# Optimization experiments

Hardware: AMD Instinct MI355X
Metric: run time of the kernel (lower is better)

## Reference

```python
import jax, jax.numpy as jnp
import numpy as np

N_EMBED = 1024
N_HEAD = 16
SEQ = 2048
BATCH = 2


def setup_inputs() -> dict:
    key = jax.random.key(0)
    ks = jax.random.split(key, 5)
    scale_in = 1.0 / np.sqrt(N_EMBED)
    x = jax.random.normal(ks[0], (BATCH, SEQ, N_EMBED), dtype=jnp.float32)
    # attn_proj: Linear(n_embed, 3*n_embed); stored as [in, out] so y = x @ W + b
    W_qkv = jax.random.normal(ks[1], (N_EMBED, 3 * N_EMBED), dtype=jnp.float32) * scale_in
    b_qkv = jax.random.normal(ks[2], (3 * N_EMBED,), dtype=jnp.float32) * 0.01
    # fin_proj: Linear(n_embed, n_embed)
    W_out = jax.random.normal(ks[3], (N_EMBED, N_EMBED), dtype=jnp.float32) * scale_in
    b_out = jax.random.normal(ks[4], (N_EMBED,), dtype=jnp.float32) * 0.01
    return {"x": x, "W_qkv": W_qkv, "b_qkv": b_qkv, "W_out": W_out, "b_out": b_out}


def reference(x, W_qkv, b_qkv, W_out, b_out):
    B, S, D = x.shape
    H = N_HEAD
    hd = D // H
    qkv = x @ W_qkv + b_qkv  # [B, S, 3D]
    q, k, v = jnp.split(qkv, 3, axis=-1)
    # [B, H, S, hd]
    q = q.reshape(B, S, H, hd).transpose(0, 2, 1, 3)
    k = k.reshape(B, S, H, hd).transpose(0, 2, 1, 3)
    v = v.reshape(B, S, H, hd).transpose(0, 2, 1, 3)
    scores = jnp.einsum("bhqd,bhkd->bhqk", q, k) * (1.0 / np.sqrt(hd))
    causal = jnp.tril(jnp.ones((S, S), dtype=bool))  # lower-triangular mask
    scores = jnp.where(causal[None, None], scores, -jnp.inf)
    probs = jax.nn.softmax(scores, axis=-1)
    # dropout is identity in eval mode (inference reference)
    attn = jnp.einsum("bhqk,bhkd->bhqd", probs, v)  # [B, H, S, hd]
    attn = attn.transpose(0, 2, 1, 3).reshape(B, S, D)
    return attn @ W_out + b_out
```

## Files before the change

kernel.cpp:

```cpp
#include <hip/hip_runtime.h>

typedef short bf16x8 __attribute__((ext_vector_type(8)));
typedef short bf16x4 __attribute__((ext_vector_type(4)));
typedef float f32x4 __attribute__((ext_vector_type(4)));
typedef int i32x4 __attribute__((ext_vector_type(4)));
typedef int i32x2 __attribute__((ext_vector_type(2)));

#define MFMA16x16x32(a, b, c) __builtin_amdgcn_mfma_f32_16x16x32_bf16(a, b, c, 0, 0, 0)
#define TRR(dst, a) asm volatile("ds_read_b64_tr_b16 %0, %1" : "=v"(dst) : "v"(a))

__device__ __forceinline__ unsigned short f2bf(float f) {
  union { float f; unsigned u; } v; v.f = f;
  unsigned u = v.u + 0x7FFFu + ((v.u >> 16) & 1u);
  return (unsigned short)(u >> 16);
}

__device__ __forceinline__ unsigned cvtpk(float lo, float hi) {
  unsigned r;
  asm("v_cvt_pk_bf16_f32 %0, %1, %2" : "=v"(r) : "v"(lo), "v"(hi));
  return r;
}

__device__ __forceinline__ float max3f(float a, float b, float c) {
  float d;
  asm("v_max3_f32 %0, %1, %2, %3" : "=v"(d) : "v"(a), "v"(b), "v"(c));
  return d;
}

__device__ __forceinline__ void gload16(const void* g, void* l) {
  __builtin_amdgcn_global_load_lds((const __attribute__((address_space(1))) void*)g,
                                   (__attribute__((address_space(3))) void*)l, 16, 0, 0);
}

__device__ __forceinline__ unsigned ldsoff(const void* p) {
  return (unsigned)(unsigned long long)(const __attribute__((address_space(3))) void*)p;
}

__global__ __launch_bounds__(256) void conv_bf16(const float* __restrict__ in,
                                                 unsigned short* __restrict__ out, int n8) {
  int i = blockIdx.x * 256 + threadIdx.x;
  if (i >= n8) return;
  const float4* p = reinterpret_cast<const float4*>(in + (long)i * 8);
  float4 a = p[0], b = p[1];
  i32x4 o;
  o[0] = cvtpk(a.x, a.y); o[1] = cvtpk(a.z, a.w);
  o[2] = cvtpk(b.x, b.y); o[3] = cvtpk(b.z, b.w);
  *reinterpret_cast<i32x4*>(out + (long)i * 8) = o;
}

__global__ __launch_bounds__(256) void trans_f32_bf16(const float* __restrict__ W,
                                                      unsigned short* __restrict__ Wt,
                                                      int K, int N) {
  __shared__ float tile[32][33];
  int n0 = blockIdx.x << 5, k0 = blockIdx.y << 5;
  int tx = threadIdx.x, ty = threadIdx.y;
#pragma unroll
  for (int i = 0; i < 32; i += 8)
    tile[ty + i][tx] = W[(long)(k0 + ty + i) * N + n0 + tx];
  __syncthreads();
#pragma unroll
  for (int i = 0; i < 32; i += 8)
    Wt[(long)(n0 + ty + i) * K + k0 + tx] = f2bf(tile[tx][ty + i]);
}

template <int BF16OUT>
__global__ __launch_bounds__(256) void gemm_bt(const unsigned short* __restrict__ A,
                                               const unsigned short* __restrict__ Bt,
                                               const float* __restrict__ bias,
                                               void* __restrict__ Cv,
                                               int M, int N, int K) {
  __shared__ __align__(128) unsigned short As[4096];
  __shared__ __align__(128) unsigned short Bs[4096];
  int t = threadIdx.x;
  int w = t >> 6, l = t & 63;
  int g = l >> 4, m16 = l & 15;
  int wr = w >> 1, wc = w & 1;
  long am0 = (long)blockIdx.y << 7;
  long bn0 = (long)blockIdx.x << 7;
  f32x4 acc[4][4];
#pragma unroll
  for (int i = 0; i < 4; ++i)
#pragma unroll
    for (int j = 0; j < 4; ++j) acc[i][j] = (f32x4){0.f, 0.f, 0.f, 0.f};

  for (int k0 = 0; k0 < K; k0 += 32) {
#pragma unroll
    for (int i = 0; i < 2; ++i) {
      int seg = i * 4 + w;
      int flat = (seg << 9) + (l << 3);
      int r_ = flat >> 5, c_ = flat & 31;
      gload16(A + (am0 + r_) * K + k0 + c_, &As[seg << 9]);
      gload16(Bt + (bn0 + r_) * K + k0 + c_, &Bs[seg << 9]);
    }
    __syncthreads();
    bf16x8 af[4], bfr[4];
#pragma unroll
    for (int im = 0; im < 4; ++im)
      af[im] = *(const bf16x8*)&As[((wr << 6) + (im << 4) + m16) * 32 + (g << 3)];
#pragma unroll
    for (int in = 0; in < 4; ++in)
      bfr[in] = *(const bf16x8*)&Bs[((wc << 6) + (in << 4) + m16) * 32 + (g << 3)];
    __builtin_amdgcn_s_setprio(1);
#pragma unroll
    for (int im = 0; im < 4; ++im)
#pragma unroll
      for (int in = 0; in < 4; ++in)
        acc[im][in] = MFMA16x16x32(af[im], bfr[in], acc[im][in]);
    __builtin_amdgcn_s_setprio(0);
    __syncthreads();
  }

#pragma unroll
  for (int im = 0; im < 4; ++im) {
#pragma unroll
    for (int in = 0; in < 4; ++in) {
      long col = bn0 + (wc << 6) + (in << 4) + m16;
      float bval = bias[col];
#pragma unroll
      for (int r = 0; r < 4; ++r) {
        long row = am0 + (wr << 6) + (im << 4) + (g << 2) + r;
        float v = acc[im][in][r] + bval;
        if (BF16OUT)
          ((unsigned short*)Cv)[row * N + col] = f2bf(v);
        else
          ((float*)Cv)[row * N + col] = v;
      }
    }
  }
}

__global__ __launch_bounds__(256, 2) void attn_fwd(const unsigned short* __restrict__ qkv,
                                                   unsigned short* __restrict__ out) {
  const int D3 = 3072;
  const float C1 = 0.18033688f;
  const float THR = 11.5415603f;
  __shared__ __align__(128) unsigned short Ks[2][8192];
  __shared__ __align__(128) unsigned short Vs[2][8192];
  int b = blockIdx.x >> 4, h = blockIdx.x & 15;
  int t = threadIdx.x;
  int w = t >> 6, l = t & 63;
  int g = l >> 4, m16 = l & 15;
  long base = (long)b * 2048 * D3;
  const unsigned short* kbase = qkv + base + 1024 + h * 64;
  const unsigned short* vbase = qkv + base + 2048 + h * 64;

  int l8 = l >> 3, sc = l & 7;
  int kof = (w * 8 + l8) * D3 + ((sc ^ l8) << 3);
  int vof = ((w * 8 + l8) * 4 + (sc >> 1)) * D3 + ((sc & 1) << 3);
  const f32x4 zero4 = (f32x4){0.f, 0.f, 0.f, 0.f};

  for (int sgi = 0; sgi < 2; ++sgi) {
    int qt = sgi ? (31 - blockIdx.y) : blockIdx.y;
    int q0 = qt << 6;
    int qrow = q0 + (w << 4) + m16;
    const unsigned short* qp = qkv + base + (long)qrow * D3 + h * 64;
    bf16x8 qf0 = *(const bf16x8*)(qp + g * 8);
    bf16x8 qf1 = *(const bf16x8*)(qp + 32 + g * 8);

    f32x4 O[4];
#pragma unroll
    for (int d = 0; d < 4; ++d) O[d] = zero4;
    float m2 = -1e30f, lsum = 0.f;
    int nt = (qt >> 1) + 1;

#pragma unroll
    for (int i = 0; i < 4; ++i) {
      gload16(kbase + kof + i * 32 * D3, &Ks[0][(i << 11) + (w << 9)]);
      gload16(vbase + vof + (i << 4), &Vs[0][(i << 11) + (w << 9)]);
    }
    __syncthreads();

    int buf = 0;
    for (int it = 0; it < nt; ++it) {
      if (it + 1 < nt) {
        long off = (long)(it + 1) * 128 * D3;
#pragma unroll
        for (int i = 0; i < 4; ++i) {
          gload16(kbase + off + kof + i * 32 * D3, &Ks[buf ^ 1][(i << 11) + (w << 9)]);
          gload16(vbase + off + vof + (i << 4), &Vs[buf ^ 1][(i << 11) + (w << 9)]);
        }
      }
      unsigned va = ldsoff(&Vs[buf][0]) + (g << 7) + (m16 << 3);
      bf16x4 tLo[4][4], tHi[4][4];
#pragma unroll
      for (int G = 0; G < 4; ++G)
#pragma unroll
        for (int d = 0; d < 4; ++d) {
          unsigned a = va + (G << 10) + (d << 12);
          TRR(tLo[G][d], a);
          TRR(tHi[G][d], a + 512);
        }
      const char* kbuf = (const char*)&Ks[buf][0];
      int swz = m16 & 7;
      f32x4 st[8];
      __builtin_amdgcn_s_setprio(1);
#pragma unroll
      for (int T = 0; T < 8; ++T) {
        const char* rp = kbuf + (((T << 4) + m16) << 7);
        bf16x8 kf0 = *(const bf16x8*)(rp + ((g ^ swz) << 4));
        bf16x8 kf1 = *(const bf16x8*)(rp + (((4 + g) ^ swz) << 4));
        st[T] = MFMA16x16x32(kf0, qf0, zero4);
        st[T] = MFMA16x16x32(kf1, qf1, st[T]);
      }
      __builtin_amdgcn_s_setprio(0);

      if (it == nt - 1) {
        int rq = qrow - (it << 7);
#pragma unroll
        for (int T = 0; T < 8; ++T)
#pragma unroll
          for (int r = 0; r < 4; ++r)
            if ((T << 4) + (g << 2) + r > rq) st[T][r] = -3e38f;
      }
      float tm[8];
#pragma unroll
      for (int T = 0; T < 8; ++T)
        tm[T] = max3f(fmaxf(st[T][0], st[T][1]), st[T][2], st[T][3]);
      float u0 = max3f(tm[0], tm[1], tm[2]);
      float u1 = max3f(tm[3], tm[4], tm[5]);
      float tmax = max3f(u0, u1, fmaxf(tm[6], tm[7]));
      tmax = fmaxf(tmax, __shfl_xor(tmax, 16));
      tmax = fmaxf(tmax, __shfl_xor(tmax, 32));
      float tsc2 = tmax * C1;
      bool skip = __all(tsc2 <= m2 + THR);
      float mnew2 = skip ? m2 : fmaxf(m2, tsc2);
      float p[8][4];
      f32x4 ts4 = zero4;
#pragma unroll
      for (int T = 0; T < 8; ++T)
#pragma unroll
        for (int r = 0; r < 4; ++r) {
          float e = __builtin_amdgcn_exp2f(fmaf(st[T][r], C1, -mnew2));
          p[T][r] = e;
          ts4[r] += e;
        }
      float tsum = (ts4[0] + ts4[1]) + (ts4[2] + ts4[3]);
      tsum += __shfl_xor(tsum, 16);
      tsum += __shfl_xor(tsum, 32);
      if (!skip) {
        float alpha = __builtin_amdgcn_exp2f(m2 - mnew2);
        lsum *= alpha;
#pragma unroll
        for (int d = 0; d < 4; ++d) {
          O[d][0] *= alpha; O[d][1] *= alpha; O[d][2] *= alpha; O[d][3] *= alpha;
        }
        m2 = mnew2;
      }
      lsum += tsum;

      bf16x8 pb[4];
#pragma unroll
      for (int G = 0; G < 4; ++G) {
        i32x4 wv;
        wv[0] = cvtpk(p[2 * G][0], p[2 * G][1]);
        wv[1] = cvtpk(p[2 * G][2], p[2 * G][3]);
        wv[2] = cvtpk(p[2 * G + 1][0], p[2 * G + 1][1]);
        wv[3] = cvtpk(p[2 * G + 1][2], p[2 * G + 1][3]);
        pb[G] = __builtin_bit_cast(bf16x8, wv);
      }

      asm volatile("s_waitcnt lgkmcnt(0)" ::: "memory");
      __builtin_amdgcn_sched_barrier(0);

      __builtin_amdgcn_s_setprio(1);
#pragma unroll
      for (int d = 0; d < 4; ++d)
#pragma unroll
        for (int G = 0; G < 4; ++G) {
          bf16x8 vf = __builtin_shufflevector(tLo[G][d], tHi[G][d], 0, 1, 2, 3, 4, 5, 6, 7);
          O[d] = MFMA16x16x32(vf, pb[G], O[d]);
        }
      __builtin_amdgcn_s_setprio(0);
      __syncthreads();
      buf ^= 1;
    }

    float inv = 1.0f / lsum;
    unsigned short* op = out + (long)(b * 2048 + qrow) * 1024 + h * 64;
#pragma unroll
    for (int d = 0; d < 4; ++d) {
      i32x2 pk;
      pk[0] = (int)cvtpk(O[d][0] * inv, O[d][1] * inv);
      pk[1] = (int)cvtpk(O[d][2] * inv, O[d][3] * inv);
      *reinterpret_cast<i32x2*>(op + (d << 4) + (g << 2)) = pk;
    }
  }
}

extern "C" void kernel_launch(void* const* d_in, const int* in_sizes, int n_in,
                              void* d_out, int out_size, void* d_ws, size_t ws_size,
                              hipStream_t stream) {
  const float* x     = (const float*)d_in[0];
  const float* W_qkv = (const float*)d_in[1];
  const float* b_qkv = (const float*)d_in[2];
  const float* W_out = (const float*)d_in[3];
  const float* b_out = (const float*)d_in[4];

  char* ws = (char*)d_ws;
  unsigned short* xb    = (unsigned short*)ws;
  unsigned short* wqkvT = (unsigned short*)(ws + (8l << 20));
  unsigned short* woutT = (unsigned short*)(ws + (14l << 20));
  unsigned short* qkv   = (unsigned short*)(ws + (16l << 20));

  conv_bf16<<<2048, 256, 0, stream>>>(x, xb, 524288);
  trans_f32_bf16<<<dim3(96, 32), dim3(32, 8), 0, stream>>>(W_qkv, wqkvT, 1024, 3072);
  trans_f32_bf16<<<dim3(32, 32), dim3(32, 8), 0, stream>>>(W_out, woutT, 1024, 1024);
  gemm_bt<1><<<dim3(24, 32), 256, 0, stream>>>(xb, wqkvT, b_qkv, (void*)qkv, 4096, 3072, 1024);
  attn_fwd<<<dim3(32, 16), 256, 0, stream>>>(qkv, xb);
  gemm_bt<0><<<dim3(8, 32), 256, 0, stream>>>(xb, woutT, b_out, d_out, 4096, 1024, 1024);
}
```

Baseline: 118.2 us.

## Deepen GEMM K-tile with XCD remap; split attention q-tiles, single-buffer LDS

The GEMM now loads a 64-wide K slice per iteration instead of 32 and remaps workgroup IDs so neighbouring tiles land on the same XCD, with an explicit vmcnt wait before the barrier. The attention kernel drops the two-q-tile loop per block, launching twice as many blocks that each handle one q-tile. It also drops K/V double buffering to a single buffer so more blocks fit per CU, and defers the row-sum cross-lane reduction to the end. The intent is to cut per-iteration barrier overhead, improve L2 locality and raise occupancy. The cost is that K/V loads are no longer overlapped with compute within a block.

```diff
diff --git a/kernel.cpp b/kernel.cpp
--- a/kernel.cpp
+++ b/kernel.cpp
@@ -69,44 +69,53 @@
                                                const float* __restrict__ bias,
                                                void* __restrict__ Cv,
                                                int M, int N, int K) {
-  __shared__ __align__(128) unsigned short As[4096];
-  __shared__ __align__(128) unsigned short Bs[4096];
+  __shared__ __align__(128) unsigned short As[8192];
+  __shared__ __align__(128) unsigned short Bs[8192];
   int t = threadIdx.x;
   int w = t >> 6, l = t & 63;
   int g = l >> 4, m16 = l & 15;
   int wr = w >> 1, wc = w & 1;
-  long am0 = (long)blockIdx.y << 7;
-  long bn0 = (long)blockIdx.x << 7;
+  int nwg = gridDim.x * gridDim.y;
+  int f = blockIdx.y * gridDim.x + blockIdx.x;
+  int q8 = nwg >> 3;
+  int s = (f & 7) * q8 + (f >> 3);
+  int bx = s % gridDim.x, by = s / gridDim.x;
+  long am0 = (long)by << 7;
+  long bn0 = (long)bx << 7;
   f32x4 acc[4][4];
 #pragma unroll
   for (int i = 0; i < 4; ++i)
 #pragma unroll
     for (int j = 0; j < 4; ++j) acc[i][j] = (f32x4){0.f, 0.f, 0.f, 0.f};
 
-  for (int k0 = 0; k0 < K; k0 += 32) {
-#pragma unroll
-    for (int i = 0; i < 2; ++i) {
+  for (int k0 = 0; k0 < K; k0 += 64) {
+#pragma unroll
+    for (int i = 0; i < 4; ++i) {
       int seg = i * 4 + w;
       int flat = (seg << 9) + (l << 3);
-      int r_ = flat >> 5, c_ = flat & 31;
+      int r_ = flat >> 6, c_ = flat & 63;
       gload16(A + (am0 + r_) * K + k0 + c_, &As[seg << 9]);
       gload16(Bt + (bn0 + r_) * K + k0 + c_, &Bs[seg << 9]);
     }
+    asm volatile("s_waitcnt vmcnt(0)" ::: "memory");
     __syncthreads();
-    bf16x8 af[4], bfr[4];
-#pragma unroll
-    for (int im = 0; im < 4; ++im)
-      af[im] = *(const bf16x8*)&As[((wr << 6) + (im << 4) + m16) * 32 + (g << 3)];
-#pragma unroll
-    for (int in = 0; in < 4; ++in)
-      bfr[in] = *(const bf16x8*)&Bs[((wc << 6) + (in << 4) + m16) * 32 + (g << 3)];
-    __builtin_amdgcn_s_setprio(1);
-#pragma unroll
-    for (int im = 0; im < 4; ++im)
+#pragma unroll
+    for (int kk = 0; kk < 2; ++kk) {
+      bf16x8 af[4], bfr[4];
+#pragma unroll
+      for (int im = 0; im < 4; ++im)
+        af[im] = *(const bf16x8*)&As[((wr << 6) + (im << 4) + m16) * 64 + (kk << 5) + (g << 3)];
 #pragma unroll
       for (int in = 0; in < 4; ++in)
-        acc[im][in] = MFMA16x16x32(af[im], bfr[in], acc[im][in]);
-    __builtin_amdgcn_s_setprio(0);
+        bfr[in] = *(const bf16x8*)&Bs[((wc << 6) + (in << 4) + m16) * 64 + (kk << 5) + (g << 3)];
+      __builtin_amdgcn_s_setprio(1);
+#pragma unroll
+      for (int im = 0; im < 4; ++im)
+#pragma unroll
+        for (int in = 0; in < 4; ++in)
+          acc[im][in] = MFMA16x16x32(af[im], bfr[in], acc[im][in]);
+      __builtin_amdgcn_s_setprio(0);
+    }
     __syncthreads();
   }
 
@@ -129,14 +138,16 @@
   }
 }
 
-__global__ __launch_bounds__(256, 2) void attn_fwd(const unsigned short* __restrict__ qkv,
+__global__ __launch_bounds__(256, 3) void attn_fwd(const unsigned short* __restrict__ qkv,
                                                    unsigned short* __restrict__ out) {
   const int D3 = 3072;
   const float C1 = 0.18033688f;
   const float THR = 11.5415603f;
-  __shared__ __align__(128) unsigned short Ks[2][8192];
-  __shared__ __align__(128) unsigned short Vs[2][8192];
+  __shared__ __align__(128) unsigned short Ks[8192];
+  __shared__ __align__(128) unsigned short Vs[8192];
   int b = blockIdx.x >> 4, h = blockIdx.x & 15;
+  int yy = blockIdx.y;
+  int qt = (yy & 1) ? (31 - (yy >> 1)) : (yy >> 1);
   int t = threadIdx.x;
   int w = t >> 6, l = t & 63;
   int g = l >> 4, m16 = l & 15;
@@ -149,141 +160,128 @@
   int vof = ((w * 8 + l8) * 4 + (sc >> 1)) * D3 + ((sc & 1) << 3);
   const f32x4 zero4 = (f32x4){0.f, 0.f, 0.f, 0.f};
 
-  for (int sgi = 0; sgi < 2; ++sgi) {
-    int qt = sgi ? (31 - blockIdx.y) : blockIdx.y;
-    int q0 = qt << 6;
-    int qrow = q0 + (w << 4) + m16;
-    const unsigned short* qp = qkv + base + (long)qrow * D3 + h * 64;
-    bf16x8 qf0 = *(const bf16x8*)(qp + g * 8);
-    bf16x8 qf1 = *(const bf16x8*)(qp + 32 + g * 8);
-
-    f32x4 O[4];
-#pragma unroll
-    for (int d = 0; d < 4; ++d) O[d] = zero4;
-    float m2 = -1e30f, lsum = 0.f;
-    int nt = (qt >> 1) + 1;
-
+  int qrow = (qt << 6) + (w << 4) + m16;
+  const unsigned short* qp = qkv + base + (long)qrow * D3 + h * 64;
+  bf16x8 qf0 = *(const bf16x8*)(qp + g * 8);
+  bf16x8 qf1 = *(const bf16x8*)(qp + 32 + g * 8);
+
+  f32x4 O[4];
+#pragma unroll
+  for (int d = 0; d < 4; ++d) O[d] = zero4;
+  f32x4 lsv = zero4;
+  float m2 = -1e30f;
+  int nt = (qt >> 1) + 1;
+
+  for (int ss = 0; ss < nt; ++ss) {
+    long off = (long)ss * 128 * D3;
 #pragma unroll
     for (int i = 0; i < 4; ++i) {
-      gload16(kbase + kof + i * 32 * D3, &Ks[0][(i << 11) + (w << 9)]);
-      gload16(vbase + vof + (i << 4), &Vs[0][(i << 11) + (w << 9)]);
-    }
+      gload16(kbase + off + kof + i * 32 * D3, &Ks[(i << 11) + (w << 9)]);
+      gload16(vbase + off + vof + (i << 4), &Vs[(i << 11) + (w << 9)]);
+    }
+    asm volatile("s_waitcnt vmcnt(0)" ::: "memory");
     __syncthreads();
 
-    int buf = 0;
-    for (int it = 0; it < nt; ++it) {
-      if (it + 1 < nt) {
-        long off = (long)(it + 1) * 128 * D3;
-#pragma unroll
-        for (int i = 0; i < 4; ++i) {
-          gload16(kbase + off + kof + i * 32 * D3, &Ks[buf ^ 1][(i << 11) + (w << 9)]);
-          gload16(vbase + off + vof + (i << 4), &Vs[buf ^ 1][(i << 11) + (w << 9)]);
-        }
+    unsigned va = ldsoff(&Vs[0]) + (g << 7) + (m16 << 3);
+    bf16x4 tLo[4][4], tHi[4][4];
+#pragma unroll
+    for (int G = 0; G < 4; ++G)
+#pragma unroll
+      for (int d = 0; d < 4; ++d) {
+        unsigned a = va + (G << 10) + (d << 12);
+        TRR(tLo[G][d], a);
+        TRR(tHi[G][d], a + 512);
       }
-      unsigned va = ldsoff(&Vs[buf][0]) + (g << 7) + (m16 << 3);
-      bf16x4 tLo[4][4], tHi[4][4];
-#pragma unroll
-      for (int G = 0; G < 4; ++G)
-#pragma unroll
-        for (int d = 0; d < 4; ++d) {
-          unsigned a = va + (G << 10) + (d << 12);
-          TRR(tLo[G][d], a);
-          TRR(tHi[G][d], a + 512);
-        }
-      const char* kbuf = (const char*)&Ks[buf][0];
-      int swz = m16 & 7;
-      f32x4 st[8];
-      __builtin_amdgcn_s_setprio(1);
-#pragma unroll
-      for (int T = 0; T < 8; ++T) {
-        const char* rp = kbuf + (((T << 4) + m16) << 7);
-        bf16x8 kf0 = *(const bf16x8*)(rp + ((g ^ swz) << 4));
-        bf16x8 kf1 = *(const bf16x8*)(rp + (((4 + g) ^ swz) << 4));
-        st[T] = MFMA16x16x32(kf0, qf0, zero4);
-        st[T] = MFMA16x16x32(kf1, qf1, st[T]);
+    const char* kbuf = (const char*)&Ks[0];
+    int swz = m16 & 7;
+    f32x4 st[8];
+    __builtin_amdgcn_s_setprio(1);
+#pragma unroll
+    for (int T = 0; T < 8; ++T) {
+      const char* rp = kbuf + (((T << 4) + m16) << 7);
+      bf16x8 kf0 = *(const bf16x8*)(rp + ((g ^ swz) << 4));
+      bf16x8 kf1 = *(const bf16x8*)(rp + (((4 + g) ^ swz) << 4));
+      st[T] = MFMA16x16x32(kf0, qf0, zero4);
+      st[T] = MFMA16x16x32(kf1, qf1, st[T]);
+    }
+    __builtin_amdgcn_s_setprio(0);
+
+    if (ss == nt - 1) {
+      int rq = qrow - (ss << 7);
+#pragma unroll
+      for (int T = 0; T < 8; ++T)
+#pragma unroll
+        for (int r = 0; r < 4; ++r)
+          if ((T << 4) + (g << 2) + r > rq) st[T][r] = -3e38f;
+    }
+    float tm[8];
+#pragma unroll
+    for (int T = 0; T < 8; ++T)
+      tm[T] = max3f(fmaxf(st[T][0], st[T][1]), st[T][2], st[T][3]);
+    float u0 = max3f(tm[0], tm[1], tm[2]);
+    float u1 = max3f(tm[3], tm[4], tm[5]);
+    float tmax = max3f(u0, u1, fmaxf(tm[6], tm[7]));
+    tmax = fmaxf(tmax, __shfl_xor(tmax, 16));
+    tmax = fmaxf(tmax, __shfl_xor(tmax, 32));
+    float tsc2 = tmax * C1;
+    bool skip = __all(tsc2 <= m2 + THR);
+    float mnew2 = skip ? m2 : fmaxf(m2, tsc2);
+    float p[8][4];
+    f32x4 ts4 = zero4;
+#pragma unroll
+    for (int T = 0; T < 8; ++T)
+#pragma unroll
+      for (int r = 0; r < 4; ++r) {
+        float e = __builtin_amdgcn_exp2f(fmaf(st[T][r], C1, -mnew2));
+        p[T][r] = e;
+        ts4[r] += e;
       }
-      __builtin_amdgcn_s_setprio(0);
-
-      if (it == nt - 1) {
-        int rq = qrow - (it << 7);
-#pragma unroll
-        for (int T = 0; T < 8; ++T)
-#pragma unroll
-          for (int r = 0; r < 4; ++r)
-            if ((T << 4) + (g << 2) + r > rq) st[T][r] = -3e38f;
+    if (!skip) {
+      float alpha = __builtin_amdgcn_exp2f(m2 - mnew2);
+      lsv *= alpha;
+#pragma unroll
+      for (int d = 0; d < 4; ++d) O[d] *= alpha;
+      m2 = mnew2;
+    }
+    lsv += ts4;
+
+    bf16x8 pb[4];
+#pragma unroll
+    for (int G = 0; G < 4; ++G) {
+      i32x4 wv;
+      wv[0] = cvtpk(p[2 * G][0], p[2 * G][1]);
+      wv[1] = cvtpk(p[2 * G][2], p[2 * G][3]);
+      wv[2] = cvtpk(p[2 * G + 1][0], p[2 * G + 1][1]);
+      wv[3] = cvtpk(p[2 * G + 1][2], p[2 * G + 1][3]);
+      pb[G] = __builtin_bit_cast(bf16x8, wv);
+    }
+
+    asm volatile("s_waitcnt lgkmcnt(0)" ::: "memory");
+    __builtin_amdgcn_sched_barrier(0);
+
+    __builtin_amdgcn_s_setprio(1);
+#pragma unroll
+    for (int d = 0; d < 4; ++d)
+#pragma unroll
+      for (int G = 0; G < 4; ++G) {
+        bf16x8 vf = __builtin_shufflevector(tLo[G][d], tHi[G][d], 0, 1, 2, 3, 4, 5, 6, 7);
+        O[d] = MFMA16x16x32(vf, pb[G], O[d]);
       }
-      float tm[8];
-#pragma unroll
-      for (int T = 0; T < 8; ++T)
-        tm[T] = max3f(fmaxf(st[T][0], st[T][1]), st[T][2], st[T][3]);
-      float u0 = max3f(tm[0], tm[1], tm[2]);
-      float u1 = max3f(tm[3], tm[4], tm[5]);
-      float tmax = max3f(u0, u1, fmaxf(tm[6], tm[7]));
-      tmax = fmaxf(tmax, __shfl_xor(tmax, 16));
-      tmax = fmaxf(tmax, __shfl_xor(tmax, 32));
-      float tsc2 = tmax * C1;
-      bool skip = __all(tsc2 <= m2 + THR);
-      float mnew2 = skip ? m2 : fmaxf(m2, tsc2);
-      float p[8][4];
-      f32x4 ts4 = zero4;
-#pragma unroll
-      for (int T = 0; T < 8; ++T)
-#pragma unroll
-        for (int r = 0; r < 4; ++r) {
-          float e = __builtin_amdgcn_exp2f(fmaf(st[T][r], C1, -mnew2));
-          p[T][r] = e;
-          ts4[r] += e;
-        }
-      float tsum = (ts4[0] + ts4[1]) + (ts4[2] + ts4[3]);
-      tsum += __shfl_xor(tsum, 16);
-      tsum += __shfl_xor(tsum, 32);
-      if (!skip) {
-        float alpha = __builtin_amdgcn_exp2f(m2 - mnew2);
-        lsum *= alpha;
-#pragma unroll
-        for (int d = 0; d < 4; ++d) {
-          O[d][0] *= alpha; O[d][1] *= alpha; O[d][2] *= alpha; O[d][3] *= alpha;
-        }
-        m2 = mnew2;
-      }
-      lsum += tsum;
-
-      bf16x8 pb[4];
-#pragma unroll
-      for (int G = 0; G < 4; ++G) {
-        i32x4 wv;
-        wv[0] = cvtpk(p[2 * G][0], p[2 * G][1]);
-        wv[1] = cvtpk(p[2 * G][2], p[2 * G][3]);
-        wv[2] = cvtpk(p[2 * G + 1][0], p[2 * G + 1][1]);
-        wv[3] = cvtpk(p[2 * G + 1][2], p[2 * G + 1][3]);
-        pb[G] = __builtin_bit_cast(bf16x8, wv);
-      }
-
-      asm volatile("s_waitcnt lgkmcnt(0)" ::: "memory");
-      __builtin_amdgcn_sched_barrier(0);
-
-      __builtin_amdgcn_s_setprio(1);
-#pragma unroll
-      for (int d = 0; d < 4; ++d)
-#pragma unroll
-        for (int G = 0; G < 4; ++G) {
-          bf16x8 vf = __builtin_shufflevector(tLo[G][d], tHi[G][d], 0, 1, 2, 3, 4, 5, 6, 7);
-          O[d] = MFMA16x16x32(vf, pb[G], O[d]);
-        }
-      __builtin_amdgcn_s_setprio(0);
-      __syncthreads();
-      buf ^= 1;
-    }
-
-    float inv = 1.0f / lsum;
-    unsigned short* op = out + (long)(b * 2048 + qrow) * 1024 + h * 64;
-#pragma unroll
-    for (int d = 0; d < 4; ++d) {
-      i32x2 pk;
-      pk[0] = (int)cvtpk(O[d][0] * inv, O[d][1] * inv);
-      pk[1] = (int)cvtpk(O[d][2] * inv, O[d][3] * inv);
-      *reinterpret_cast<i32x2*>(op + (d << 4) + (g << 2)) = pk;
-    }
+    __builtin_amdgcn_s_setprio(0);
+    __syncthreads();
+  }
+
+  float s = (lsv[0] + lsv[1]) + (lsv[2] + lsv[3]);
+  s += __shfl_xor(s, 16);
+  s += __shfl_xor(s, 32);
+  float inv = 1.0f / s;
+  unsigned short* op = out + (long)(b * 2048 + qrow) * 1024 + h * 64;
+#pragma unroll
+  for (int d = 0; d < 4; ++d) {
+    i32x2 pk;
+    pk[0] = (int)cvtpk(O[d][0] * inv, O[d][1] * inv);
+    pk[1] = (int)cvtpk(O[d][2] * inv, O[d][3] * inv);
+    *reinterpret_cast<i32x2*>(op + (d << 4) + (g << 2)) = pk;
   }
 }
 
@@ -306,6 +304,6 @@
   trans_f32_bf16<<<dim3(96, 32), dim3(32, 8), 0, stream>>>(W_qkv, wqkvT, 1024, 3072);
   trans_f32_bf16<<<dim3(32, 32), dim3(32, 8), 0, stream>>>(W_out, woutT, 1024, 1024);
   gemm_bt<1><<<dim3(24, 32), 256, 0, stream>>>(xb, wqkvT, b_qkv, (void*)qkv, 4096, 3072, 1024);
-  attn_fwd<<<dim3(32, 16), 256, 0, stream>>>(qkv, xb);
+  attn_fwd<<<dim3(32, 32), 256, 0, stream>>>(qkv, xb);
   gemm_bt<0><<<dim3(8, 32), 256, 0, stream>>>(xb, woutT, b_out, d_out, 4096, 1024, 1024);
 }
```

Result: slower. 121.7 us (+2.9%).
